# Performance work log

Hardware: AMD Instinct MI355X
Metric: run time of the kernel (lower is better)

Reference implementation:

```python
import jax, jax.numpy as jnp
import numpy as np

NUM_HEADS = 8
NUM_GROUPS = 32
EPS = 1e-5


def group_norm(x, gamma, beta):
    # x: [B, C, H, W]; normalize over (C//G, H, W) within each of G groups
    B, C, H, W = x.shape
    xg = x.reshape(B, NUM_GROUPS, C // NUM_GROUPS, H, W)
    mean = xg.mean(axis=(2, 3, 4), keepdims=True)
    var = xg.var(axis=(2, 3, 4), keepdims=True)
    xn = ((xg - mean) * jax.lax.rsqrt(var + EPS)).reshape(B, C, H, W)
    return xn * gamma[None, :, None, None] + beta[None, :, None, None]


def setup_inputs() -> dict:
    key = jax.random.key(0)
    ks = jax.random.split(key, 7)
    B, C, H, W = 16, 512, 32, 32
    x = jax.random.normal(ks[0], (B, C, H, W), dtype=jnp.float32)
    gamma = jnp.ones((C,), dtype=jnp.float32)
    beta = jnp.zeros((C,), dtype=jnp.float32)
    # 1x1 convs == per-pixel linear layers
    w_qkv = jax.random.normal(ks[1], (3 * C, C), dtype=jnp.float32) * (1.0 / np.sqrt(C))
    b_qkv = jax.random.normal(ks[2], (3 * C,), dtype=jnp.float32) * 0.02
    w_proj = jax.random.normal(ks[3], (C, C), dtype=jnp.float32) * (1.0 / np.sqrt(C))
    b_proj = jax.random.normal(ks[4], (C,), dtype=jnp.float32) * 0.02
    return {"x": x, "gamma": gamma, "beta": beta, "w_qkv": w_qkv,
            "b_qkv": b_qkv, "w_proj": w_proj, "b_proj": b_proj}


def reference(x, gamma, beta, w_qkv, b_qkv, w_proj, b_proj):
    B, C, H, W = x.shape
    nh = NUM_HEADS
    d = C // nh
    N = H * W
    h = group_norm(x, gamma, beta)
    # 1x1 conv: [B,C,H,W] x [3C,C] -> [B,3C,H,W]
    qkv = jnp.einsum('bchw,oc->bohw', h, w_qkv) + b_qkv[None, :, None, None]
    qkv = qkv.reshape(B, 3, nh, d, N)  # matches torch reshape(B,3,heads,d,HW)
    q, k, v = qkv[:, 0], qkv[:, 1], qkv[:, 2]
    scale = d ** (-0.5)
    attn = jnp.einsum('bhdn,bhdm->bhnm', q, k) * scale  # [B,h,N,N]
    attn = jax.nn.softmax(attn, axis=-1)
    out = jnp.einsum('bhnm,bhdm->bhdn', attn, v)  # [B,h,d,N]
    out = out.reshape(B, C, H, W)
    proj = jnp.einsum('bchw,oc->bohw', out, w_proj) + b_proj[None, :, None, None]
    return x + proj
```

## Files before the change

kernel.cpp:

```cpp
#include <hip/hip_runtime.h>
#include <cstddef>

#define B_  16
#define C_  512
#define N_  1024
#define QSC 0.18033688011112042f

typedef __attribute__((ext_vector_type(8))) __bf16 bf16x8;
typedef __attribute__((ext_vector_type(4))) float f32x4;

__device__ __forceinline__ unsigned short f2bf(float x) {
  unsigned u = __float_as_uint(x);
  return (unsigned short)((u + 0x7fffu + ((u >> 16) & 1u)) >> 16);
}

#define GLDS16(g, l)                                                            \
  __builtin_amdgcn_global_load_lds(                                             \
      (const __attribute__((address_space(1))) void*)(g),                       \
      (__attribute__((address_space(3))) void*)(l), 16, 0, 0)

__global__ __launch_bounds__(256) void wconv_kernel(
    const float* __restrict__ wq, const float* __restrict__ wp,
    unsigned short* __restrict__ oq, unsigned short* __restrict__ op) {
  int i = blockIdx.x * 256 + threadIdx.x;
  const float4* src; unsigned short* dst; int off;
  if (i < 196608) { src = (const float4*)wq; dst = oq; off = i; }
  else            { src = (const float4*)wp; dst = op; off = i - 196608; }
  float4 v = src[off];
  union { unsigned short s[4]; ushort4 u; } o;
  o.s[0] = f2bf(v.x); o.s[1] = f2bf(v.y);
  o.s[2] = f2bf(v.z); o.s[3] = f2bf(v.w);
  *(ushort4*)(dst + (size_t)off * 4) = o.u;
}

__global__ __launch_bounds__(256) void gn_kernel(
    const float* __restrict__ x, const float* __restrict__ gamma,
    const float* __restrict__ beta, unsigned short* __restrict__ hT) {
  int bg = blockIdx.x;
  int b = bg >> 5, g = bg & 31;
  size_t base = ((size_t)b * C_ + (size_t)g * 16) * N_;
  const float4* x4 = (const float4*)(x + base);
  int tid = threadIdx.x;

  float sum = 0.f, sq = 0.f;
  float4 vv[16];
#pragma unroll
  for (int i = 0; i < 16; i++) {
    float4 v = x4[tid + i * 256];
    vv[i] = v;
    sum += v.x + v.y + v.z + v.w;
    sq  += v.x * v.x + v.y * v.y + v.z * v.z + v.w * v.w;
  }
#pragma unroll
  for (int off = 32; off > 0; off >>= 1) {
    sum += __shfl_down(sum, off, 64);
    sq  += __shfl_down(sq, off, 64);
  }
  __shared__ float sm[4], sv[4];
  int lane = tid & 63, w = tid >> 6;
  if (lane == 0) { sm[w] = sum; sv[w] = sq; }
  __syncthreads();
  if (tid == 0) {
    float s = sm[0] + sm[1] + sm[2] + sm[3];
    float q = sv[0] + sv[1] + sv[2] + sv[3];
    float mean = s * (1.f / 16384.f);
    float var  = q * (1.f / 16384.f) - mean * mean;
    sm[0] = mean;
    sv[0] = rsqrtf(var + 1e-5f);
  }
  __syncthreads();
  float mean = sm[0], rstd = sv[0];

  union { unsigned short s[16]; uint4 u[2]; } row[4];
#pragma unroll
  for (int i = 0; i < 16; i++) {
    int c = g * 16 + i;
    float ga = gamma[c] * rstd;
    float be = beta[c] - mean * ga;
    float4 v = vv[i];
    row[0].s[i] = f2bf(v.x * ga + be);
    row[1].s[i] = f2bf(v.y * ga + be);
    row[2].s[i] = f2bf(v.z * ga + be);
    row[3].s[i] = f2bf(v.w * ga + be);
  }
#pragma unroll
  for (int j = 0; j < 4; j++) {
    uint4* dst = (uint4*)(hT + ((size_t)b * N_ + 4 * tid + j) * C_ + g * 16);
    dst[0] = row[j].u[0];
    dst[1] = row[j].u[1];
  }
}

template <int MODE>
__global__ __launch_bounds__(256) void gemm_mfma(
    const unsigned short* __restrict__ Wb, const float* __restrict__ bias,
    const unsigned short* __restrict__ InT, const float* __restrict__ resid,
    void* __restrict__ Out, void* __restrict__ Out2, int M) {
  __shared__ __align__(16) unsigned short As[128 * 32];
  __shared__ __align__(16) unsigned short Bs[128 * 32];

  const int b = blockIdx.z;
  const int n0 = blockIdx.x * 128, m0 = blockIdx.y * 128;
  const int tid = threadIdx.x;
  const int lane = tid & 63, wave = tid >> 6;
  const int col = lane & 15, quad = lane >> 4;
  const int wm = (wave >> 1) << 6, wn = (wave & 1) << 6;

  const unsigned short* Ag = Wb + (size_t)m0 * C_;
  const unsigned short* Bg = InT + ((size_t)b * N_ + n0) * C_;

  const int r0 = tid >> 2, c0 = (tid & 3) << 3;

  f32x4 acc[4][4];
#pragma unroll
  for (int i = 0; i < 4; i++)
#pragma unroll
    for (int j = 0; j < 4; j++) acc[i][j] = f32x4{0.f, 0.f, 0.f, 0.f};

  for (int k0 = 0; k0 < C_; k0 += 32) {
    __syncthreads();
    GLDS16(Ag + (size_t)r0 * C_ + k0 + c0,        &As[tid * 8]);
    GLDS16(Ag + (size_t)(r0 + 64) * C_ + k0 + c0, &As[(tid + 256) * 8]);
    GLDS16(Bg + (size_t)r0 * C_ + k0 + c0,        &Bs[tid * 8]);
    GLDS16(Bg + (size_t)(r0 + 64) * C_ + k0 + c0, &Bs[(tid + 256) * 8]);
    __syncthreads();

    bf16x8 af[4], bfr[4];
#pragma unroll
    for (int mt = 0; mt < 4; mt++)
      af[mt] = *(const bf16x8*)&As[(wm + mt * 16 + col) * 32 + quad * 8];
#pragma unroll
    for (int nt = 0; nt < 4; nt++)
      bfr[nt] = *(const bf16x8*)&Bs[(wn + nt * 16 + col) * 32 + quad * 8];
#pragma unroll
    for (int mt = 0; mt < 4; mt++)
#pragma unroll
      for (int nt = 0; nt < 4; nt++)
        acc[mt][nt] = __builtin_amdgcn_mfma_f32_16x16x32_bf16(
            af[mt], bfr[nt], acc[mt][nt], 0, 0, 0);
  }

  if constexpr (MODE == 0) {
#pragma unroll
    for (int mt = 0; mt < 4; mt++) {
      int mbase = m0 + wm + mt * 16 + quad * 4;
#pragma unroll
      for (int nt = 0; nt < 4; nt++) {
        int n = n0 + wn + nt * 16 + col;
#pragma unroll
        for (int r = 0; r < 4; r++) {
          int m = mbase + r;
          size_t off = ((size_t)b * M + m) * N_ + n;
          ((float*)Out)[off] = acc[mt][nt][r] + bias[m] + resid[off];
        }
      }
    }
  } else {
    if (blockIdx.y < 8) {
      float qs = (blockIdx.y < 4) ? QSC : 1.0f;
#pragma unroll
      for (int mt = 0; mt < 4; mt++) {
        int mbase = m0 + wm + mt * 16 + quad * 4;
#pragma unroll
        for (int nt = 0; nt < 4; nt++) {
          int n = n0 + wn + nt * 16 + col;
          union { unsigned short s[4]; ushort4 v; } o;
#pragma unroll
          for (int r = 0; r < 4; r++)
            o.s[r] = f2bf((acc[mt][nt][r] + bias[mbase + r]) * qs);
          *(ushort4*)((unsigned short*)Out + ((size_t)b * N_ + n) * 1024 + mbase) = o.v;
        }
      }
    } else {
#pragma unroll
      for (int mt = 0; mt < 4; mt++) {
        int mbase = m0 + wm + mt * 16 + quad * 4;
#pragma unroll
        for (int nt = 0; nt < 4; nt++) {
          int n = n0 + wn + nt * 16 + col;
#pragma unroll
          for (int r = 0; r < 4; r++) {
            int m = mbase + r;
            ((unsigned short*)Out2)[((size_t)b * 512 + (m - 1024)) * N_ + n] =
                f2bf(acc[mt][nt][r] + bias[m]);
          }
        }
      }
    }
  }
}

__global__ __launch_bounds__(256) void attn_mfma(
    const unsigned short* __restrict__ qkT, const unsigned short* __restrict__ Vb,
    unsigned short* __restrict__ aoT) {
  __shared__ __align__(16) unsigned short Vs[2][64 * 64];

  const int tid = threadIdx.x;
  const int wave = tid >> 6, lane = tid & 63;
  const int quad = lane >> 4, col = lane & 15;
  const int b = blockIdx.z, hh = blockIdx.y;
  const int qblk = blockIdx.x * 256 + wave * 64;

  const unsigned short* qkrow = qkT + (size_t)b * N_ * 1024;
  const unsigned short* vp = Vb + ((size_t)b * 512 + hh * 64) * N_;

  bf16x8 qf[4][2];
#pragma unroll
  for (int nt = 0; nt < 4; nt++) {
    const unsigned short* qr = qkrow + (size_t)(qblk + nt * 16 + col) * 1024 + hh * 64;
#pragma unroll
    for (int ks = 0; ks < 2; ks++)
      qf[nt][ks] = *(const bf16x8*)(qr + ks * 32 + quad * 8);
  }

  const int krow_base = 8 * (col >> 2) + (col & 3);

  float l_i[4];
  f32x4 O[4][4];
#pragma unroll
  for (int nt = 0; nt < 4; nt++) {
    l_i[nt] = 0.f;
#pragma unroll
    for (int mt = 0; mt < 4; mt++) O[mt][nt] = f32x4{0.f, 0.f, 0.f, 0.f};
  }

  const int sd = tid >> 3, ss = tid & 7;
  const int sc0 = (ss ^ (sd & 7)) * 8;
  const int sc1 = (ss ^ ((sd + 32) & 7)) * 8;

#define STAGE_V(p, kt)                                                          \
  do {                                                                          \
    GLDS16(vp + (size_t)sd * N_ + (kt) * 64 + sc0, &Vs[p][tid * 8]);            \
    GLDS16(vp + (size_t)(sd + 32) * N_ + (kt) * 64 + sc1,                       \
           &Vs[p][(tid + 256) * 8]);                                            \
  } while (0)

  STAGE_V(0, 0);

  for (int kt = 0; kt < 16; kt++) {
    const int p = kt & 1;
    __syncthreads();
    if (kt < 15) STAGE_V(p ^ 1, kt + 1);

    bf16x8 kf[4][2];
#pragma unroll
    for (int u = 0; u < 4; u++) {
      int krow = kt * 64 + 32 * (u >> 1) + 4 * (u & 1) + krow_base;
      const unsigned short* kr = qkrow + (size_t)krow * 1024 + 512 + hh * 64;
#pragma unroll
      for (int ks = 0; ks < 2; ks++)
        kf[u][ks] = *(const bf16x8*)(kr + ks * 32 + quad * 8);
    }

    bf16x8 vf[4][2];
#pragma unroll
    for (int mt = 0; mt < 4; mt++) {
      int d = 16 * mt + col;
#pragma unroll
      for (int s = 0; s < 2; s++)
        vf[mt][s] = *(const bf16x8*)&Vs[p][d * 64 + (((4 * s + quad) ^ (d & 7)) << 3)];
    }

#pragma unroll
    for (int nt = 0; nt < 4; nt++) {
#pragma unroll
      for (int s = 0; s < 2; s++) {
        f32x4 sfA = f32x4{0.f, 0.f, 0.f, 0.f};
        f32x4 sfB = f32x4{0.f, 0.f, 0.f, 0.f};
#pragma unroll
        for (int ks = 0; ks < 2; ks++) {
          sfA = __builtin_amdgcn_mfma_f32_16x16x32_bf16(kf[2 * s][ks], qf[nt][ks], sfA, 0, 0, 0);
          sfB = __builtin_amdgcn_mfma_f32_16x16x32_bf16(kf[2 * s + 1][ks], qf[nt][ks], sfB, 0, 0, 0);
        }
        float eA0 = __builtin_amdgcn_exp2f(sfA[0]);
        float eA1 = __builtin_amdgcn_exp2f(sfA[1]);
        float eA2 = __builtin_amdgcn_exp2f(sfA[2]);
        float eA3 = __builtin_amdgcn_exp2f(sfA[3]);
        float eB0 = __builtin_amdgcn_exp2f(sfB[0]);
        float eB1 = __builtin_amdgcn_exp2f(sfB[1]);
        float eB2 = __builtin_amdgcn_exp2f(sfB[2]);
        float eB3 = __builtin_amdgcn_exp2f(sfB[3]);
        l_i[nt] += ((eA0 + eA1) + (eA2 + eA3)) + ((eB0 + eB1) + (eB2 + eB3));
        union { unsigned u[4]; bf16x8 v; } pf;
        pf.u[0] = __builtin_amdgcn_perm(__float_as_uint(eA1), __float_as_uint(eA0), 0x07060302u);
        pf.u[1] = __builtin_amdgcn_perm(__float_as_uint(eA3), __float_as_uint(eA2), 0x07060302u);
        pf.u[2] = __builtin_amdgcn_perm(__float_as_uint(eB1), __float_as_uint(eB0), 0x07060302u);
        pf.u[3] = __builtin_amdgcn_perm(__float_as_uint(eB3), __float_as_uint(eB2), 0x07060302u);
#pragma unroll
        for (int mt = 0; mt < 4; mt++)
          O[mt][nt] = __builtin_amdgcn_mfma_f32_16x16x32_bf16(vf[mt][s], pf.v, O[mt][nt], 0, 0, 0);
      }
    }
  }

#pragma unroll
  for (int nt = 0; nt < 4; nt++) {
    float ls = l_i[nt];
    ls += __shfl_xor(ls, 16, 64);
    ls += __shfl_xor(ls, 32, 64);
    float inv = 1.f / ls;
    int qg = qblk + nt * 16 + col;
    unsigned short* dst = aoT + ((size_t)b * N_ + qg) * C_ + hh * 64;
#pragma unroll
    for (int mt = 0; mt < 4; mt++) {
      union { unsigned short s[4]; ushort4 v; } o;
#pragma unroll
      for (int r = 0; r < 4; r++) o.s[r] = f2bf(O[mt][nt][r] * inv);
      *(ushort4*)(dst + mt * 16 + quad * 4) = o.v;
    }
  }
#undef STAGE_V
}

extern "C" void kernel_launch(void* const* d_in, const int* in_sizes, int n_in,
                              void* d_out, int out_size, void* d_ws, size_t ws_size,
                              hipStream_t stream) {
  (void)in_sizes; (void)n_in; (void)out_size; (void)ws_size;
  const float* x      = (const float*)d_in[0];
  const float* gamma  = (const float*)d_in[1];
  const float* beta   = (const float*)d_in[2];
  const float* w_qkv  = (const float*)d_in[3];
  const float* b_qkv  = (const float*)d_in[4];
  const float* w_proj = (const float*)d_in[5];
  const float* b_proj = (const float*)d_in[6];
  float* out = (float*)d_out;

  unsigned short* hT  = (unsigned short*)d_ws;
  unsigned short* qkT = hT + (size_t)B_ * N_ * C_;
  unsigned short* Vb  = qkT + (size_t)B_ * N_ * 1024;
  unsigned short* aoT = hT;
  unsigned short* wqb = Vb + (size_t)B_ * C_ * N_;
  unsigned short* wpb = wqb + (size_t)1536 * 512;

  wconv_kernel<<<dim3(1024), dim3(256), 0, stream>>>(w_qkv, w_proj, wqb, wpb);
  gn_kernel<<<dim3(B_ * 32), dim3(256), 0, stream>>>(x, gamma, beta, hT);
  gemm_mfma<1><<<dim3(8, 12, 16), dim3(256), 0, stream>>>(
      wqb, b_qkv, hT, (const float*)nullptr, (void*)qkT, (void*)Vb, 1536);
  attn_mfma<<<dim3(4, 8, 16), dim3(256), 0, stream>>>(qkT, Vb, aoT);
  gemm_mfma<0><<<dim3(8, 4, 16), dim3(256), 0, stream>>>(
      wpb, b_proj, aoT, x, (void*)out, (void*)nullptr, 512);
}
```

Measured before the change: 240.0 us.

## Prefetch K fragments, compute softmax row sums via MFMA, stage QK output through LDS

The attention loop is unrolled by two with ping-pong K register buffers, so the global K loads for the next tile are issued before the current tile is computed. This hides load latency at the cost of more VGPRs. The softmax denominator now comes from an extra MFMA against a ones vector, which replaces per-lane scalar adds and the cross-lane shuffles. The QK GEMM epilogue transposes its output through padded shared memory so each thread writes 16-byte coalesced stores instead of scattered 8-byte ones. This adds LDS use and two barriers.

```diff
diff --git a/kernel.cpp b/kernel.cpp
--- a/kernel.cpp
+++ b/kernel.cpp
@@ -96,8 +96,9 @@
     const unsigned short* __restrict__ Wb, const float* __restrict__ bias,
     const unsigned short* __restrict__ InT, const float* __restrict__ resid,
     void* __restrict__ Out, void* __restrict__ Out2, int M) {
-  __shared__ __align__(16) unsigned short As[128 * 32];
-  __shared__ __align__(16) unsigned short Bs[128 * 32];
+  __shared__ __align__(16) unsigned short smem[(MODE == 1) ? 128 * 136 : 8192];
+  unsigned short* As = smem;
+  unsigned short* Bs = smem + 4096;
 
   const int b = blockIdx.z;
   const int n0 = blockIdx.x * 128, m0 = blockIdx.y * 128;
@@ -158,18 +159,28 @@
   } else {
     if (blockIdx.y < 8) {
       float qs = (blockIdx.y < 4) ? QSC : 1.0f;
+      __syncthreads();
 #pragma unroll
       for (int mt = 0; mt < 4; mt++) {
-        int mbase = m0 + wm + mt * 16 + quad * 4;
+        int lm = wm + mt * 16 + quad * 4;
 #pragma unroll
         for (int nt = 0; nt < 4; nt++) {
-          int n = n0 + wn + nt * 16 + col;
+          int ln = wn + nt * 16 + col;
           union { unsigned short s[4]; ushort4 v; } o;
 #pragma unroll
           for (int r = 0; r < 4; r++)
-            o.s[r] = f2bf((acc[mt][nt][r] + bias[mbase + r]) * qs);
-          *(ushort4*)((unsigned short*)Out + ((size_t)b * N_ + n) * 1024 + mbase) = o.v;
+            o.s[r] = f2bf((acc[mt][nt][r] + bias[m0 + lm + r]) * qs);
+          *(ushort4*)&smem[ln * 136 + lm] = o.v;
         }
+      }
+      __syncthreads();
+      const int c = tid & 15, rr = tid >> 4;
+#pragma unroll
+      for (int i = 0; i < 8; i++) {
+        int row = rr + i * 16;
+        uint4 v = *(const uint4*)&smem[row * 136 + c * 8];
+        *(uint4*)((unsigned short*)Out +
+                  ((size_t)b * N_ + n0 + row) * 1024 + m0 + c * 8) = v;
       }
     } else {
 #pragma unroll
@@ -215,14 +226,17 @@
 
   const int krow_base = 8 * (col >> 2) + (col & 3);
 
-  float l_i[4];
-  f32x4 O[4][4];
+  f32x4 O[4][4], lacc[4];
 #pragma unroll
   for (int nt = 0; nt < 4; nt++) {
-    l_i[nt] = 0.f;
+    lacc[nt] = f32x4{0.f, 0.f, 0.f, 0.f};
 #pragma unroll
     for (int mt = 0; mt < 4; mt++) O[mt][nt] = f32x4{0.f, 0.f, 0.f, 0.f};
   }
+
+  union { unsigned short s[8]; bf16x8 v; } one8;
+#pragma unroll
+  for (int j = 0; j < 8; j++) one8.s[j] = 0x3F80;
 
   const int sd = tid >> 3, ss = tid & 7;
   const int sc0 = (ss ^ (sd & 7)) * 8;
@@ -235,70 +249,74 @@
            &Vs[p][(tid + 256) * 8]);                                            \
   } while (0)
 
+#define LOADK(dst, kt)                                                          \
+  do {                                                                          \
+    _Pragma("unroll")                                                           \
+    for (int u = 0; u < 4; u++) {                                               \
+      int krow = (kt) * 64 + 32 * (u >> 1) + 4 * (u & 1) + krow_base;           \
+      const unsigned short* kr = qkrow + (size_t)krow * 1024 + 512 + hh * 64;   \
+      dst[u][0] = *(const bf16x8*)(kr + quad * 8);                              \
+      dst[u][1] = *(const bf16x8*)(kr + 32 + quad * 8);                         \
+    }                                                                           \
+  } while (0)
+
+#define TILE(kt, P, KC, KN)                                                     \
+  do {                                                                          \
+    __syncthreads();                                                            \
+    if ((kt) < 15) { STAGE_V((P) ^ 1, (kt) + 1); LOADK(KN, (kt) + 1); }         \
+    bf16x8 vf[4][2];                                                            \
+    _Pragma("unroll")                                                           \
+    for (int mt = 0; mt < 4; mt++) {                                            \
+      int d = 16 * mt + col;                                                    \
+      _Pragma("unroll")                                                         \
+      for (int s = 0; s < 2; s++)                                               \
+        vf[mt][s] = *(const bf16x8*)&Vs[P][d * 64 + (((4 * s + quad) ^ (d & 7)) << 3)]; \
+    }                                                                           \
+    _Pragma("unroll")                                                           \
+    for (int nt = 0; nt < 4; nt++) {                                            \
+      _Pragma("unroll")                                                         \
+      for (int s = 0; s < 2; s++) {                                             \
+        f32x4 sfA = f32x4{0.f, 0.f, 0.f, 0.f};                                  \
+        f32x4 sfB = f32x4{0.f, 0.f, 0.f, 0.f};                                  \
+        _Pragma("unroll")                                                       \
+        for (int ks = 0; ks < 2; ks++) {                                        \
+          sfA = __builtin_amdgcn_mfma_f32_16x16x32_bf16(KC[2 * s][ks], qf[nt][ks], sfA, 0, 0, 0);     \
+          sfB = __builtin_amdgcn_mfma_f32_16x16x32_bf16(KC[2 * s + 1][ks], qf[nt][ks], sfB, 0, 0, 0); \
+        }                                                                       \
+        float eA0 = __builtin_amdgcn_exp2f(sfA[0]);                             \
+        float eA1 = __builtin_amdgcn_exp2f(sfA[1]);                             \
+        float eA2 = __builtin_amdgcn_exp2f(sfA[2]);                             \
+        float eA3 = __builtin_amdgcn_exp2f(sfA[3]);                             \
+        float eB0 = __builtin_amdgcn_exp2f(sfB[0]);                             \
+        float eB1 = __builtin_amdgcn_exp2f(sfB[1]);                             \
+        float eB2 = __builtin_amdgcn_exp2f(sfB[2]);                             \
+        float eB3 = __builtin_amdgcn_exp2f(sfB[3]);                             \
+        union { unsigned u[4]; bf16x8 v; } pf;                                  \
+        pf.u[0] = __builtin_amdgcn_perm(__float_as_uint(eA1), __float_as_uint(eA0), 0x07060302u); \
+        pf.u[1] = __builtin_amdgcn_perm(__float_as_uint(eA3), __float_as_uint(eA2), 0x07060302u); \
+        pf.u[2] = __builtin_amdgcn_perm(__float_as_uint(eB1), __float_as_uint(eB0), 0x07060302u); \
+        pf.u[3] = __builtin_amdgcn_perm(__float_as_uint(eB3), __float_as_uint(eB2), 0x07060302u); \
+        lacc[nt] = __builtin_amdgcn_mfma_f32_16x16x32_bf16(one8.v, pf.v, lacc[nt], 0, 0, 0);      \
+        _Pragma("unroll")                                                       \
+        for (int mt = 0; mt < 4; mt++)                                          \
+          O[mt][nt] = __builtin_amdgcn_mfma_f32_16x16x32_bf16(vf[mt][s], pf.v, O[mt][nt], 0, 0, 0); \
+      }                                                                         \
+    }                                                                           \
+  } while (0)
+
+  bf16x8 kfa[4][2], kfb[4][2];
+  LOADK(kfa, 0);
   STAGE_V(0, 0);
 
-  for (int kt = 0; kt < 16; kt++) {
-    const int p = kt & 1;
-    __syncthreads();
-    if (kt < 15) STAGE_V(p ^ 1, kt + 1);
-
-    bf16x8 kf[4][2];
-#pragma unroll
-    for (int u = 0; u < 4; u++) {
-      int krow = kt * 64 + 32 * (u >> 1) + 4 * (u & 1) + krow_base;
-      const unsigned short* kr = qkrow + (size_t)krow * 1024 + 512 + hh * 64;
-#pragma unroll
-      for (int ks = 0; ks < 2; ks++)
-        kf[u][ks] = *(const bf16x8*)(kr + ks * 32 + quad * 8);
-    }
-
-    bf16x8 vf[4][2];
-#pragma unroll
-    for (int mt = 0; mt < 4; mt++) {
-      int d = 16 * mt + col;
-#pragma unroll
-      for (int s = 0; s < 2; s++)
-        vf[mt][s] = *(const bf16x8*)&Vs[p][d * 64 + (((4 * s + quad) ^ (d & 7)) << 3)];
-    }
-
-#pragma unroll
-    for (int nt = 0; nt < 4; nt++) {
-#pragma unroll
-      for (int s = 0; s < 2; s++) {
-        f32x4 sfA = f32x4{0.f, 0.f, 0.f, 0.f};
-        f32x4 sfB = f32x4{0.f, 0.f, 0.f, 0.f};
-#pragma unroll
-        for (int ks = 0; ks < 2; ks++) {
-          sfA = __builtin_amdgcn_mfma_f32_16x16x32_bf16(kf[2 * s][ks], qf[nt][ks], sfA, 0, 0, 0);
-          sfB = __builtin_amdgcn_mfma_f32_16x16x32_bf16(kf[2 * s + 1][ks], qf[nt][ks], sfB, 0, 0, 0);
-        }
-        float eA0 = __builtin_amdgcn_exp2f(sfA[0]);
-        float eA1 = __builtin_amdgcn_exp2f(sfA[1]);
-        float eA2 = __builtin_amdgcn_exp2f(sfA[2]);
-        float eA3 = __builtin_amdgcn_exp2f(sfA[3]);
-        float eB0 = __builtin_amdgcn_exp2f(sfB[0]);
-        float eB1 = __builtin_amdgcn_exp2f(sfB[1]);
-        float eB2 = __builtin_amdgcn_exp2f(sfB[2]);
-        float eB3 = __builtin_amdgcn_exp2f(sfB[3]);
-        l_i[nt] += ((eA0 + eA1) + (eA2 + eA3)) + ((eB0 + eB1) + (eB2 + eB3));
-        union { unsigned u[4]; bf16x8 v; } pf;
-        pf.u[0] = __builtin_amdgcn_perm(__float_as_uint(eA1), __float_as_uint(eA0), 0x07060302u);
-        pf.u[1] = __builtin_amdgcn_perm(__float_as_uint(eA3), __float_as_uint(eA2), 0x07060302u);
-        pf.u[2] = __builtin_amdgcn_perm(__float_as_uint(eB1), __float_as_uint(eB0), 0x07060302u);
-        pf.u[3] = __builtin_amdgcn_perm(__float_as_uint(eB3), __float_as_uint(eB2), 0x07060302u);
-#pragma unroll
-        for (int mt = 0; mt < 4; mt++)
-          O[mt][nt] = __builtin_amdgcn_mfma_f32_16x16x32_bf16(vf[mt][s], pf.v, O[mt][nt], 0, 0, 0);
-      }
-    }
+#pragma unroll 1
+  for (int kt2 = 0; kt2 < 8; kt2++) {
+    TILE(2 * kt2, 0, kfa, kfb);
+    TILE(2 * kt2 + 1, 1, kfb, kfa);
   }
 
 #pragma unroll
   for (int nt = 0; nt < 4; nt++) {
-    float ls = l_i[nt];
-    ls += __shfl_xor(ls, 16, 64);
-    ls += __shfl_xor(ls, 32, 64);
-    float inv = 1.f / ls;
+    float inv = 1.f / lacc[nt][0];
     int qg = qblk + nt * 16 + col;
     unsigned short* dst = aoT + ((size_t)b * N_ + qg) * C_ + hh * 64;
 #pragma unroll
@@ -310,6 +328,8 @@
     }
   }
 #undef STAGE_V
+#undef LOADK
+#undef TILE
 }
 
 extern "C" void kernel_launch(void* const* d_in, const int* in_sizes, int n_in,
```

Measured after the change: 239.3 us. About the same (-0.3%).

## Halve attention query tile, drop V LDS staging, MFMA row-sums, coalesce QK store

Applied to the files above, without the earlier changes.

The attention kernel now handles 32 queries per wave, launching twice as many blocks. It drops the LDS double-buffered V staging and reads V fragments straight from global memory. The softmax denominator is now computed by an MFMA against a ones vector instead of scalar adds plus cross-lane shuffles. The QKV GEMM epilogue stages the q/k tile through shared memory so global stores are coalesced 16-byte rows, at the cost of extra LDS and barriers. Together these trade per-wave reuse and the V prefetch for more parallelism and fewer register/VALU costs.

```diff
diff --git a/kernel.cpp b/kernel.cpp
--- a/kernel.cpp
+++ b/kernel.cpp
@@ -96,8 +96,9 @@
     const unsigned short* __restrict__ Wb, const float* __restrict__ bias,
     const unsigned short* __restrict__ InT, const float* __restrict__ resid,
     void* __restrict__ Out, void* __restrict__ Out2, int M) {
-  __shared__ __align__(16) unsigned short As[128 * 32];
-  __shared__ __align__(16) unsigned short Bs[128 * 32];
+  __shared__ __align__(16) unsigned short smem[(MODE == 1) ? 128 * 136 : 8192];
+  unsigned short* As = smem;
+  unsigned short* Bs = smem + 4096;
 
   const int b = blockIdx.z;
   const int n0 = blockIdx.x * 128, m0 = blockIdx.y * 128;
@@ -158,18 +159,28 @@
   } else {
     if (blockIdx.y < 8) {
       float qs = (blockIdx.y < 4) ? QSC : 1.0f;
+      __syncthreads();
 #pragma unroll
       for (int mt = 0; mt < 4; mt++) {
-        int mbase = m0 + wm + mt * 16 + quad * 4;
+        int lm = wm + mt * 16 + quad * 4;
 #pragma unroll
         for (int nt = 0; nt < 4; nt++) {
-          int n = n0 + wn + nt * 16 + col;
+          int ln = wn + nt * 16 + col;
           union { unsigned short s[4]; ushort4 v; } o;
 #pragma unroll
           for (int r = 0; r < 4; r++)
-            o.s[r] = f2bf((acc[mt][nt][r] + bias[mbase + r]) * qs);
-          *(ushort4*)((unsigned short*)Out + ((size_t)b * N_ + n) * 1024 + mbase) = o.v;
+            o.s[r] = f2bf((acc[mt][nt][r] + bias[m0 + lm + r]) * qs);
+          *(ushort4*)&smem[ln * 136 + lm] = o.v;
         }
+      }
+      __syncthreads();
+      const int c = tid & 15, rr = tid >> 4;
+#pragma unroll
+      for (int i = 0; i < 8; i++) {
+        int row = rr + i * 16;
+        uint4 v = *(const uint4*)&smem[row * 136 + c * 8];
+        *(uint4*)((unsigned short*)Out +
+                  ((size_t)b * N_ + n0 + row) * 1024 + m0 + c * 8) = v;
       }
     } else {
 #pragma unroll
@@ -193,20 +204,18 @@
 __global__ __launch_bounds__(256) void attn_mfma(
     const unsigned short* __restrict__ qkT, const unsigned short* __restrict__ Vb,
     unsigned short* __restrict__ aoT) {
-  __shared__ __align__(16) unsigned short Vs[2][64 * 64];
-
   const int tid = threadIdx.x;
   const int wave = tid >> 6, lane = tid & 63;
   const int quad = lane >> 4, col = lane & 15;
   const int b = blockIdx.z, hh = blockIdx.y;
-  const int qblk = blockIdx.x * 256 + wave * 64;
+  const int qblk = blockIdx.x * 128 + wave * 32;
 
   const unsigned short* qkrow = qkT + (size_t)b * N_ * 1024;
   const unsigned short* vp = Vb + ((size_t)b * 512 + hh * 64) * N_;
 
-  bf16x8 qf[4][2];
-#pragma unroll
-  for (int nt = 0; nt < 4; nt++) {
+  bf16x8 qf[2][2];
+#pragma unroll
+  for (int nt = 0; nt < 2; nt++) {
     const unsigned short* qr = qkrow + (size_t)(qblk + nt * 16 + col) * 1024 + hh * 64;
 #pragma unroll
     for (int ks = 0; ks < 2; ks++)
@@ -215,33 +224,20 @@
 
   const int krow_base = 8 * (col >> 2) + (col & 3);
 
-  float l_i[4];
-  f32x4 O[4][4];
-#pragma unroll
-  for (int nt = 0; nt < 4; nt++) {
-    l_i[nt] = 0.f;
+  f32x4 O[4][2], lacc[2];
+#pragma unroll
+  for (int nt = 0; nt < 2; nt++) {
+    lacc[nt] = f32x4{0.f, 0.f, 0.f, 0.f};
 #pragma unroll
     for (int mt = 0; mt < 4; mt++) O[mt][nt] = f32x4{0.f, 0.f, 0.f, 0.f};
   }
 
-  const int sd = tid >> 3, ss = tid & 7;
-  const int sc0 = (ss ^ (sd & 7)) * 8;
-  const int sc1 = (ss ^ ((sd + 32) & 7)) * 8;
-
-#define STAGE_V(p, kt)                                                          \
-  do {                                                                          \
-    GLDS16(vp + (size_t)sd * N_ + (kt) * 64 + sc0, &Vs[p][tid * 8]);            \
-    GLDS16(vp + (size_t)(sd + 32) * N_ + (kt) * 64 + sc1,                       \
-           &Vs[p][(tid + 256) * 8]);                                            \
-  } while (0)
-
-  STAGE_V(0, 0);
-
+  union { unsigned short s[8]; bf16x8 v; } one8;
+#pragma unroll
+  for (int j = 0; j < 8; j++) one8.s[j] = 0x3F80;
+
+#pragma unroll 2
   for (int kt = 0; kt < 16; kt++) {
-    const int p = kt & 1;
-    __syncthreads();
-    if (kt < 15) STAGE_V(p ^ 1, kt + 1);
-
     bf16x8 kf[4][2];
 #pragma unroll
     for (int u = 0; u < 4; u++) {
@@ -251,18 +247,17 @@
       for (int ks = 0; ks < 2; ks++)
         kf[u][ks] = *(const bf16x8*)(kr + ks * 32 + quad * 8);
     }
-
     bf16x8 vf[4][2];
 #pragma unroll
     for (int mt = 0; mt < 4; mt++) {
-      int d = 16 * mt + col;
+      const unsigned short* vr = vp + (size_t)(16 * mt + col) * N_ + kt * 64;
 #pragma unroll
       for (int s = 0; s < 2; s++)
-        vf[mt][s] = *(const bf16x8*)&Vs[p][d * 64 + (((4 * s + quad) ^ (d & 7)) << 3)];
-    }
-
-#pragma unroll
-    for (int nt = 0; nt < 4; nt++) {
+        vf[mt][s] = *(const bf16x8*)(vr + 32 * s + quad * 8);
+    }
+
+#pragma unroll
+    for (int nt = 0; nt < 2; nt++) {
 #pragma unroll
       for (int s = 0; s < 2; s++) {
         f32x4 sfA = f32x4{0.f, 0.f, 0.f, 0.f};
@@ -280,12 +275,12 @@
         float eB1 = __builtin_amdgcn_exp2f(sfB[1]);
         float eB2 = __builtin_amdgcn_exp2f(sfB[2]);
         float eB3 = __builtin_amdgcn_exp2f(sfB[3]);
-        l_i[nt] += ((eA0 + eA1) + (eA2 + eA3)) + ((eB0 + eB1) + (eB2 + eB3));
         union { unsigned u[4]; bf16x8 v; } pf;
         pf.u[0] = __builtin_amdgcn_perm(__float_as_uint(eA1), __float_as_uint(eA0), 0x07060302u);
         pf.u[1] = __builtin_amdgcn_perm(__float_as_uint(eA3), __float_as_uint(eA2), 0x07060302u);
         pf.u[2] = __builtin_amdgcn_perm(__float_as_uint(eB1), __float_as_uint(eB0), 0x07060302u);
         pf.u[3] = __builtin_amdgcn_perm(__float_as_uint(eB3), __float_as_uint(eB2), 0x07060302u);
+        lacc[nt] = __builtin_amdgcn_mfma_f32_16x16x32_bf16(one8.v, pf.v, lacc[nt], 0, 0, 0);
 #pragma unroll
         for (int mt = 0; mt < 4; mt++)
           O[mt][nt] = __builtin_amdgcn_mfma_f32_16x16x32_bf16(vf[mt][s], pf.v, O[mt][nt], 0, 0, 0);
@@ -294,11 +289,8 @@
   }
 
 #pragma unroll
-  for (int nt = 0; nt < 4; nt++) {
-    float ls = l_i[nt];
-    ls += __shfl_xor(ls, 16, 64);
-    ls += __shfl_xor(ls, 32, 64);
-    float inv = 1.f / ls;
+  for (int nt = 0; nt < 2; nt++) {
+    float inv = 1.f / lacc[nt][0];
     int qg = qblk + nt * 16 + col;
     unsigned short* dst = aoT + ((size_t)b * N_ + qg) * C_ + hh * 64;
 #pragma unroll
@@ -309,7 +301,6 @@
       *(ushort4*)(dst + mt * 16 + quad * 4) = o.v;
     }
   }
-#undef STAGE_V
 }
 
 extern "C" void kernel_launch(void* const* d_in, const int* in_sizes, int n_in,
@@ -336,7 +327,7 @@
   gn_kernel<<<dim3(B_ * 32), dim3(256), 0, stream>>>(x, gamma, beta, hT);
   gemm_mfma<1><<<dim3(8, 12, 16), dim3(256), 0, stream>>>(
       wqb, b_qkv, hT, (const float*)nullptr, (void*)qkT, (void*)Vb, 1536);
-  attn_mfma<<<dim3(4, 8, 16), dim3(256), 0, stream>>>(qkT, Vb, aoT);
+  attn_mfma<<<dim3(8, 8, 16), dim3(256), 0, stream>>>(qkT, Vb, aoT);
   gemm_mfma<0><<<dim3(8, 4, 16), dim3(256), 0, stream>>>(
       wpb, b_proj, aoT, x, (void*)out, (void*)nullptr, 512);
 }
```

Result: slower. 277.1 us (+15.5%).
